# Performance work log

Hardware: AMD Instinct MI355X
Metric: run time of the kernel (lower is better)

Reference implementation:

```python
import jax, jax.numpy as jnp
import numpy as np

N_OBJ = 100000
E = 64
SMOOTH = 12.0  # MAXIMUM_SMOOTHNESS


def _mish(x):
    return x * jnp.tanh(jax.nn.softplus(x))


def _mlp(x, wi, bi, wo, bo):
    # torch.nn.Linear convention: y = x @ W.T + b
    return jnp.dot(_mish(jnp.dot(x, wi.T) + bi), wo.T) + bo


def _linear_init(key, out_dim, in_dim):
    s = 1.0 / np.sqrt(in_dim)
    kw, kb = jax.random.split(key)
    w = jax.random.uniform(kw, (out_dim, in_dim), jnp.float32, -s, s)
    b = jax.random.uniform(kb, (out_dim,), jnp.float32, -s, s)
    return w, b


def setup_inputs() -> dict:
    key = jax.random.key(0)
    ks = jax.random.split(key, 16)
    inp = {}
    inp["object_embeddings"] = jax.random.normal(ks[0], (N_OBJ, E), jnp.float32)
    inp["idx_unary"] = jax.random.randint(ks[1], (200000,), 0, N_OBJ, jnp.int32)
    inp["idx_binary"] = jax.random.randint(ks[2], (600000,), 0, N_OBJ, jnp.int32)
    inp["idx_ternary"] = jax.random.randint(ks[3], (300000,), 0, N_OBJ, jnp.int32)
    k = 4
    for name, ar in [("unary", 1), ("binary", 2), ("ternary", 3)]:
        d = ar * E
        wi, bi = _linear_init(ks[k], d, d)
        wo, bo = _linear_init(ks[k + 1], d, d)
        inp[f"{name}_wi"], inp[f"{name}_bi"] = wi, bi
        inp[f"{name}_wo"], inp[f"{name}_bo"] = wo, bo
        k += 2
    # update MLP: Linear(2E,2E) then Linear(2E,E)
    inp["upd_wi"], inp["upd_bi"] = _linear_init(ks[k], 2 * E, 2 * E)
    inp["upd_wo"], inp["upd_bo"] = _linear_init(ks[k + 1], E, 2 * E)
    return inp


def reference(object_embeddings, idx_unary, idx_binary, idx_ternary,
              unary_wi, unary_bi, unary_wo, unary_bo,
              binary_wi, binary_bi, binary_wo, binary_bo,
              ternary_wi, ternary_bi, ternary_wo, ternary_bo,
              upd_wi, upd_bi, upd_wo, upd_bo):
    def rel_msg(idx, arity, wi, bi, wo, bo):
        x = object_embeddings[idx].reshape(-1, arity * E)  # gather
        m = x + _mlp(x, wi, bi, wo, bo)                    # residual per-relation MLP
        return m.reshape(-1, E)

    msgs = jnp.concatenate([
        rel_msg(idx_unary, 1, unary_wi, unary_bi, unary_wo, unary_bo),
        rel_msg(idx_binary, 2, binary_wi, binary_bi, binary_wo, binary_bo),
        rel_msg(idx_ternary, 3, ternary_wi, ternary_bi, ternary_wo, ternary_bo),
    ], axis=0)
    inds = jnp.concatenate([idx_unary, idx_binary, idx_ternary], axis=0)

    # scatter-amax (include_self=False -> untouched rows stay 0, like torch zeros init)
    mx = jax.ops.segment_max(msgs, inds, num_segments=N_OBJ)
    mx = jnp.where(jnp.isneginf(mx), 0.0, mx)
    mx = jax.lax.stop_gradient(mx)

    exps = jnp.exp(SMOOTH * (msgs - mx[inds]))
    s = jax.ops.segment_sum(exps, inds, num_segments=N_OBJ) + 1e-16
    max_msg = jnp.log(s) / SMOOTH + mx  # smooth log-sum-exp aggregation

    upd_in = jnp.concatenate([max_msg, object_embeddings], axis=1)
    return object_embeddings + _mlp(upd_in, upd_wi, upd_bi, upd_wo, upd_bo)
```

## Files before the change

kernel.cpp:

```cpp
#include <hip/hip_runtime.h>
#include <math.h>

#define NOBJ 100000
#define SMOOTH 12.0f

typedef __attribute__((ext_vector_type(8))) short bf16x8;
typedef __attribute__((ext_vector_type(4))) float f32x4;
typedef unsigned short u16;
typedef unsigned int u32;
typedef unsigned long long u64;

#define OFF_UWI 0
#define OFF_UWO 4096
#define OFF_BWI 8192
#define OFF_BWO 24576
#define OFF_TWI 40960
#define OFF_TWO 77824
#define OFF_PWI 114688
#define OFF_PWO 131072
#define WTOT    139264
__device__ u16 g_wbf[WTOT];

__device__ __forceinline__ u16 f2b(float x) {
    union { float f; u32 u; } v; v.f = x;
    u32 r = v.u + 0x7FFFu + ((v.u >> 16) & 1);
    return (u16)(r >> 16);
}
__device__ __forceinline__ float b2f(u16 b) {
    union { u32 u; float f; } v; v.u = ((u32)b) << 16; return v.f;
}
__device__ __forceinline__ float mish_fast(float x) {
    float e = __expf(fminf(x, 15.f));
    float t = __builtin_fmaf(e, e, 2.f * e);
    return x * t * __builtin_amdgcn_rcpf(t + 2.f);
}
__device__ __forceinline__ double exp12_f64(float m) {
    float t = m * (SMOOTH * 1.4426950408889634f);
    float n = floorf(t);
    float f = exp2f(t - n);
    return ldexp((double)f, (int)n);
}
__device__ __forceinline__ float lse_from_sum(double S) {
    if (S == 0.0) return -3.0701134573253942f;
    union { double d; u64 u; } vu; vu.d = S;
    int k = (int)((vu.u >> 52) & 0x7FF) - 1022;
    vu.u = (vu.u & 0x000FFFFFFFFFFFFFULL) | 0x3FE0000000000000ULL;
    float fr = (float)vu.d;
    return ((float)k + __log2f(fr)) * 0.057762265046662105f;
}

__global__ void prep_kernel(const float* __restrict__ uwi, const float* __restrict__ uwo,
                            const float* __restrict__ bwi, const float* __restrict__ bwo,
                            const float* __restrict__ twi, const float* __restrict__ two_,
                            const float* __restrict__ pwi, const float* __restrict__ pwo,
                            const float* __restrict__ emb, u16* __restrict__ emb_bf,
                            u32* __restrict__ counts, u32* __restrict__ cursor) {
    int i = blockIdx.x * 256 + threadIdx.x;
    if (i < WTOT) {
        const float* src; int off;
        if      (i < OFF_UWO) { src = uwi; off = OFF_UWI; }
        else if (i < OFF_BWI) { src = uwo; off = OFF_UWO; }
        else if (i < OFF_BWO) { src = bwi; off = OFF_BWI; }
        else if (i < OFF_TWI) { src = bwo; off = OFF_BWO; }
        else if (i < OFF_TWO) { src = twi; off = OFF_TWI; }
        else if (i < OFF_PWI) { src = two_; off = OFF_TWO; }
        else if (i < OFF_PWO) { src = pwi; off = OFF_PWI; }
        else                  { src = pwo; off = OFF_PWO; }
        g_wbf[i] = f2b(src[i - off]);
    }
    if (i < NOBJ * 16) {
        float4 v = ((const float4*)emb)[i];
        ushort4 o;
        o.x = f2b(v.x); o.y = f2b(v.y); o.z = f2b(v.z); o.w = f2b(v.w);
        ((ushort4*)emb_bf)[i] = o;
    }
    if (counts && i < NOBJ) { counts[i] = 0u; cursor[i] = 0u; }
}

__device__ __forceinline__ int lookup_obj(long long m,
                                          const int* __restrict__ iu, int nU,
                                          const int* __restrict__ ib, int nB,
                                          const int* __restrict__ it) {
    if (m < nU) return iu[m];
    m -= nU;
    if (m < nB) return ib[m];
    return it[m - nB];
}

__global__ void hist_kernel(const int* __restrict__ iu, int nU,
                            const int* __restrict__ ib, int nB,
                            const int* __restrict__ it, int nT,
                            u32* __restrict__ counts) {
    long long t = (long long)blockIdx.x * 256 + threadIdx.x;
    if (t >= (long long)nU + nB + nT) return;
    atomicAdd(&counts[lookup_obj(t, iu, nU, ib, nB, it)], 1u);
}

__global__ void scan1_kernel(const u32* __restrict__ counts, u32* __restrict__ offs,
                             u32* __restrict__ bsum) {
    __shared__ u32 s[256];
    int t = threadIdx.x;
    int g = blockIdx.x * 256 + t;
    u32 v = (g < NOBJ) ? counts[g] : 0u;
    s[t] = v; __syncthreads();
    for (int off = 1; off < 256; off <<= 1) {
        u32 x = (t >= off) ? s[t - off] : 0u; __syncthreads();
        s[t] += x; __syncthreads();
    }
    if (g < NOBJ) offs[g] = s[t] - v;
    if (t == 255) bsum[blockIdx.x] = s[255];
}

__global__ void scan2_kernel(u32* __restrict__ bsum, int nblk) {
    __shared__ u32 s[512];
    int t = threadIdx.x;
    u32 v = (t < nblk) ? bsum[t] : 0u;
    s[t] = v; __syncthreads();
    for (int off = 1; off < 512; off <<= 1) {
        u32 x = (t >= off) ? s[t - off] : 0u; __syncthreads();
        s[t] += x; __syncthreads();
    }
    if (t < nblk) bsum[t] = s[t] - v;
}

__global__ void slot_kernel(const int* __restrict__ iu, int nU,
                            const int* __restrict__ ib, int nB,
                            const int* __restrict__ it, int nT,
                            const u32* __restrict__ offs, const u32* __restrict__ bsum,
                            u32* __restrict__ cursor, u32* __restrict__ slotByRef) {
    long long t = (long long)blockIdx.x * 256 + threadIdx.x;
    if (t >= (long long)nU + nB + nT) return;
    int obj = lookup_obj(t, iu, nU, ib, nB, it);
    u32 pos = atomicAdd(&cursor[obj], 1u);
    slotByRef[t] = offs[obj] + bsum[obj >> 8] + pos;
}

template<int D, int MW, int MODE, int WOFF_I, int WOFF_O>
__global__ __launch_bounds__(64 * MW)
void rel_pass_mfma(const u16* __restrict__ emb_bf,
                   const int* __restrict__ idx, int nRows,
                   const float* __restrict__ bi, const float* __restrict__ bo,
                   double* __restrict__ ssum64,
                   u16* __restrict__ msgs_out, const u32* __restrict__ slotByRef,
                   long long baseRef) {
    constexpr int ARITY = D / 64;
    constexpr int NT = D / 16;
    constexpr int NSC = D / 64;
    constexpr int M = MW * 16;
    __shared__ u16 xs[M * D];
    __shared__ u16 wlds[D * 64];
    __shared__ int objsm[M * ARITY];
    __shared__ u32 slotm[M * ARITY];

    const int tid = threadIdx.x;
    const int w = tid >> 6, l = tid & 63;
    const int lo = l & 15, hi = l >> 4;
    const int row0 = blockIdx.x * M;

    for (int i = tid; i < M * ARITY; i += 64 * MW) {
        int row = row0 + i / ARITY;
        bool ok = (row < nRows);
        objsm[i] = ok ? idx[(size_t)row * ARITY + i % ARITY] : -1;
        if (MODE == 3)
            slotm[i] = ok ? slotByRef[baseRef + (long long)row0 * ARITY + i] : 0xFFFFFFFFu;
    }
    __syncthreads();

    for (int i = tid; i < M * D / 8; i += 64 * MW) {
        int r = i / (D / 8), c8 = i % (D / 8);
        int obj = objsm[r * ARITY + (c8 >> 3)];
        bf16x8 v = {0, 0, 0, 0, 0, 0, 0, 0};
        if (obj >= 0) v = *(const bf16x8*)(emb_bf + (size_t)obj * 64 + (c8 & 7) * 8);
        *(bf16x8*)&xs[(r * D + c8 * 8) ^ ((r & 7) << 3)] = v;
    }

    f32x4 acc[NT];
    const int arow = w * 16 + lo;
    const int asw = (arow & 7) << 3;

#pragma unroll
    for (int n = 0; n < NT; ++n) { float b = bi[n * 16 + lo]; acc[n] = (f32x4){b, b, b, b}; }
#pragma unroll
    for (int sc = 0; sc < NSC; ++sc) {
        __syncthreads();
        for (int i = tid; i < D * 8; i += 64 * MW) {
            int u = i * 8;
            int j = u >> 6;
            bf16x8 v = *(const bf16x8*)&g_wbf[WOFF_I + j * D + sc * 64 + (u & 63)];
            *(bf16x8*)&wlds[u ^ ((j & 7) << 3)] = v;
        }
        __syncthreads();
#pragma unroll
        for (int kkL = 0; kkL < 2; ++kkL) {
            bf16x8 a = *(const bf16x8*)&xs[(arow * D + (sc * 2 + kkL) * 32 + hi * 8) ^ asw];
#pragma unroll
            for (int n = 0; n < NT; ++n) {
                int j = n * 16 + lo;
                bf16x8 b = *(const bf16x8*)&wlds[(j * 64 + kkL * 32 + hi * 8) ^ ((j & 7) << 3)];
                acc[n] = __builtin_amdgcn_mfma_f32_16x16x32_bf16(a, b, acc[n], 0, 0, 0);
            }
        }
    }

#pragma unroll
    for (int n = 0; n < NT; ++n) {
        float bov = bo[n * 16 + lo];
#pragma unroll
        for (int r = 0; r < 4; ++r) {
            int row = w * 16 + hi * 4 + r;
            int col = n * 16 + lo;
            int sidx = (row * D + col) ^ ((row & 7) << 3);
            float xv = b2f(xs[sidx]);
            xs[sidx] = f2b(mish_fast(acc[n][r]));
            acc[n][r] = bov + xv;
        }
    }

#pragma unroll
    for (int sc = 0; sc < NSC; ++sc) {
        __syncthreads();
        for (int i = tid; i < D * 8; i += 64 * MW) {
            int u = i * 8;
            int j = u >> 6;
            bf16x8 v = *(const bf16x8*)&g_wbf[WOFF_O + j * D + sc * 64 + (u & 63)];
            *(bf16x8*)&wlds[u ^ ((j & 7) << 3)] = v;
        }
        __syncthreads();
#pragma unroll
        for (int kkL = 0; kkL < 2; ++kkL) {
            bf16x8 a = *(const bf16x8*)&xs[(arow * D + (sc * 2 + kkL) * 32 + hi * 8) ^ asw];
#pragma unroll
            for (int n = 0; n < NT; ++n) {
                int j = n * 16 + lo;
                bf16x8 b = *(const bf16x8*)&wlds[(j * 64 + kkL * 32 + hi * 8) ^ ((j & 7) << 3)];
                acc[n] = __builtin_amdgcn_mfma_f32_16x16x32_bf16(a, b, acc[n], 0, 0, 0);
            }
        }
    }

    if (MODE == 3) {
#pragma unroll
        for (int n = 0; n < NT; ++n) {
            int col = n * 16 + lo;
#pragma unroll
            for (int r = 0; r < 4; ++r) {
                int row = w * 16 + hi * 4 + r;
                _Float16 hv = (_Float16)acc[n][r];
                xs[(row * D + col) ^ ((row & 7) << 3)] = *(u16*)&hv;
            }
        }
        __syncthreads();
        for (int i = tid; i < M * D / 8; i += 64 * MW) {
            int u = i * 8;
            int row = u / D, off = u - row * D;
            u32 slot = slotm[row * ARITY + (off >> 6)];
            if (slot == 0xFFFFFFFFu) continue;
            *(bf16x8*)(msgs_out + (size_t)slot * 64 + (off & 63)) =
                *(const bf16x8*)&xs[u ^ ((row & 7) << 3)];
        }
    } else {
#pragma unroll
        for (int n = 0; n < NT; ++n) {
            int col = n * 16 + lo;
#pragma unroll
            for (int r = 0; r < 4; ++r) {
                int row = w * 16 + hi * 4 + r;
                int obj = objsm[row * ARITY + (col >> 6)];
                if (obj < 0) continue;
                unsafeAtomicAdd(&ssum64[(size_t)obj * 64 + (col & 63)], exp12_f64(acc[n][r]));
            }
        }
    }
}

__global__ __launch_bounds__(256)
void agg_kernel(const u16* __restrict__ msgs,
                const u32* __restrict__ offs, const u32* __restrict__ bsum,
                const u32* __restrict__ counts,
                float* __restrict__ lse_out) {
    int o = blockIdx.x * 4 + (threadIdx.x >> 6);
    int l = threadIdx.x & 63;
    if (o >= NOBJ) return;
    u32 off = offs[o] + bsum[o >> 8];
    u32 n = counts[o];
    const u16* mrow = msgs + (size_t)off * 64 + l;
    double S0 = 0.0, S1 = 0.0, S2 = 0.0, S3 = 0.0;
    u32 j = 0;
    for (; j + 4 <= n; j += 4) {
        u16 h0 = mrow[(size_t)(j + 0) * 64];
        u16 h1 = mrow[(size_t)(j + 1) * 64];
        u16 h2 = mrow[(size_t)(j + 2) * 64];
        u16 h3 = mrow[(size_t)(j + 3) * 64];
        S0 += exp12_f64((float)(*(const _Float16*)&h0));
        S1 += exp12_f64((float)(*(const _Float16*)&h1));
        S2 += exp12_f64((float)(*(const _Float16*)&h2));
        S3 += exp12_f64((float)(*(const _Float16*)&h3));
    }
    for (; j < n; ++j) {
        u16 h = mrow[(size_t)j * 64];
        S0 += exp12_f64((float)(*(const _Float16*)&h));
    }
    lse_out[(size_t)o * 64 + l] = lse_from_sum((S0 + S1) + (S2 + S3));
}

__global__ __launch_bounds__(256)
void update_from_lse(const float* __restrict__ emb, const float* lsein,
                     const float* __restrict__ bi, const float* __restrict__ bo,
                     float* out) {
    __shared__ u16 uin[64 * 128];
    __shared__ u16 h[64 * 128];
    const int tid = threadIdx.x;
    const int w = tid >> 6, l = tid & 63, lo = l & 15, hi = l >> 4;
    const int row0 = blockIdx.x * 64;

    for (int i = tid; i < 64 * 128; i += 256) {
        int r = i >> 7, c = i & 127;
        int obj = row0 + r;
        float v = 0.f;
        if (obj < NOBJ) {
            if (c < 64) v = lsein[(size_t)obj * 64 + c];
            else v = emb[(size_t)obj * 64 + (c - 64)];
        }
        uin[i ^ ((r & 7) << 3)] = f2b(v);
    }
    __syncthreads();

    const int arow = w * 16 + lo;
    const int asw = (arow & 7) << 3;
    f32x4 acc[8];
#pragma unroll
    for (int n = 0; n < 8; ++n) { float b = bi[n * 16 + lo]; acc[n] = (f32x4){b, b, b, b}; }
#pragma unroll
    for (int kk = 0; kk < 4; ++kk) {
        bf16x8 a = *(const bf16x8*)&uin[(arow * 128 + kk * 32 + hi * 8) ^ asw];
#pragma unroll
        for (int n = 0; n < 8; ++n) {
            bf16x8 b = *(const bf16x8*)&g_wbf[OFF_PWI + (n * 16 + lo) * 128 + kk * 32 + hi * 8];
            acc[n] = __builtin_amdgcn_mfma_f32_16x16x32_bf16(a, b, acc[n], 0, 0, 0);
        }
    }
#pragma unroll
    for (int n = 0; n < 8; ++n) {
#pragma unroll
        for (int r = 0; r < 4; ++r) {
            int row = w * 16 + hi * 4 + r;
            int col = n * 16 + lo;
            h[(row * 128 + col) ^ ((row & 7) << 3)] = f2b(mish_fast(acc[n][r]));
        }
    }
    __syncthreads();
    f32x4 acc2[4];
#pragma unroll
    for (int n = 0; n < 4; ++n) { float b = bo[n * 16 + lo]; acc2[n] = (f32x4){b, b, b, b}; }
#pragma unroll
    for (int kk = 0; kk < 4; ++kk) {
        bf16x8 a = *(const bf16x8*)&h[(arow * 128 + kk * 32 + hi * 8) ^ asw];
#pragma unroll
        for (int n = 0; n < 4; ++n) {
            bf16x8 b = *(const bf16x8*)&g_wbf[OFF_PWO + (n * 16 + lo) * 128 + kk * 32 + hi * 8];
            acc2[n] = __builtin_amdgcn_mfma_f32_16x16x32_bf16(a, b, acc2[n], 0, 0, 0);
        }
    }
#pragma unroll
    for (int n = 0; n < 4; ++n) {
        int col = n * 16 + lo;
#pragma unroll
        for (int r = 0; r < 4; ++r) {
            int row = w * 16 + hi * 4 + r;
            int obj = row0 + row;
            if (obj < NOBJ)
                out[(size_t)obj * 64 + col] = emb[(size_t)obj * 64 + col] + acc2[n][r];
        }
    }
}

__global__ __launch_bounds__(256)
void update_mfma_f64(const float* __restrict__ emb, const double* __restrict__ ssum64,
                     const float* __restrict__ bi, const float* __restrict__ bo,
                     float* __restrict__ out) {
    __shared__ u16 uin[64 * 128];
    __shared__ u16 h[64 * 128];
    const int tid = threadIdx.x;
    const int w = tid >> 6, l = tid & 63, lo = l & 15, hi = l >> 4;
    const int row0 = blockIdx.x * 64;

    for (int i = tid; i < 64 * 128; i += 256) {
        int r = i >> 7, c = i & 127;
        int obj = row0 + r;
        float v = 0.f;
        if (obj < NOBJ) {
            if (c < 64) v = lse_from_sum(ssum64[(size_t)obj * 64 + c]);
            else v = emb[(size_t)obj * 64 + (c - 64)];
        }
        uin[i ^ ((r & 7) << 3)] = f2b(v);
    }
    __syncthreads();

    const int arow = w * 16 + lo;
    const int asw = (arow & 7) << 3;
    f32x4 acc[8];
#pragma unroll
    for (int n = 0; n < 8; ++n) { float b = bi[n * 16 + lo]; acc[n] = (f32x4){b, b, b, b}; }
#pragma unroll
    for (int kk = 0; kk < 4; ++kk) {
        bf16x8 a = *(const bf16x8*)&uin[(arow * 128 + kk * 32 + hi * 8) ^ asw];
#pragma unroll
        for (int n = 0; n < 8; ++n) {
            bf16x8 b = *(const bf16x8*)&g_wbf[OFF_PWI + (n * 16 + lo) * 128 + kk * 32 + hi * 8];
            acc[n] = __builtin_amdgcn_mfma_f32_16x16x32_bf16(a, b, acc[n], 0, 0, 0);
        }
    }
#pragma unroll
    for (int n = 0; n < 8; ++n) {
#pragma unroll
        for (int r = 0; r < 4; ++r) {
            int row = w * 16 + hi * 4 + r;
            int col = n * 16 + lo;
            h[(row * 128 + col) ^ ((row & 7) << 3)] = f2b(mish_fast(acc[n][r]));
        }
    }
    __syncthreads();
    f32x4 acc2[4];
#pragma unroll
    for (int n = 0; n < 4; ++n) { float b = bo[n * 16 + lo]; acc2[n] = (f32x4){b, b, b, b}; }
#pragma unroll
    for (int kk = 0; kk < 4; ++kk) {
        bf16x8 a = *(const bf16x8*)&h[(arow * 128 + kk * 32 + hi * 8) ^ asw];
#pragma unroll
        for (int n = 0; n < 4; ++n) {
            bf16x8 b = *(const bf16x8*)&g_wbf[OFF_PWO + (n * 16 + lo) * 128 + kk * 32 + hi * 8];
            acc2[n] = __builtin_amdgcn_mfma_f32_16x16x32_bf16(a, b, acc2[n], 0, 0, 0);
        }
    }
#pragma unroll
    for (int n = 0; n < 4; ++n) {
        int col = n * 16 + lo;
#pragma unroll
        for (int r = 0; r < 4; ++r) {
            int row = w * 16 + hi * 4 + r;
            int obj = row0 + row;
            if (obj < NOBJ)
                out[(size_t)obj * 64 + col] = emb[(size_t)obj * 64 + col] + acc2[n][r];
        }
    }
}

static inline size_t align256(size_t x) { return (x + 255) & ~(size_t)255; }

extern "C" void kernel_launch(void* const* d_in, const int* in_sizes, int n_in,
                              void* d_out, int out_size, void* d_ws, size_t ws_size,
                              hipStream_t stream) {
    const float* emb = (const float*)d_in[0];
    const int* iu = (const int*)d_in[1];
    const int* ib = (const int*)d_in[2];
    const int* it = (const int*)d_in[3];
    const float* uwi = (const float*)d_in[4];
    const float* ubi = (const float*)d_in[5];
    const float* uwo = (const float*)d_in[6];
    const float* ubo = (const float*)d_in[7];
    const float* bwi = (const float*)d_in[8];
    const float* bbi = (const float*)d_in[9];
    const float* bwo = (const float*)d_in[10];
    const float* bbo = (const float*)d_in[11];
    const float* twi = (const float*)d_in[12];
    const float* tbi = (const float*)d_in[13];
    const float* two_ = (const float*)d_in[14];
    const float* tbo = (const float*)d_in[15];
    const float* pwi = (const float*)d_in[16];
    const float* pbi = (const float*)d_in[17];
    const float* pwo = (const float*)d_in[18];
    const float* pbo = (const float*)d_in[19];

    const int nU = in_sizes[1];
    const int nB = in_sizes[2];
    const int nT = in_sizes[3];
    const int rowsU = nU;
    const int rowsB = nB / 2;
    const int rowsT = nT / 3;
    const long long NREF = (long long)nU + nB + nT;

    const size_t seg = (size_t)NOBJ * 64;
    const int gU = (rowsU + 127) / 128;
    const int gB = (rowsB + 127) / 128;
    const int gT = (rowsT + 127) / 128;
    const int nblkScan = (NOBJ + 255) / 256;
    const int gPrep = (NOBJ * 16 + 255) / 256;

    char* p = (char*)d_ws;
    u16* msgs = (u16*)p;        p += align256(2 * (size_t)NREF * 64);
    u32* counts = (u32*)p;      p += align256(4 * (size_t)NOBJ);
    u32* offs = (u32*)p;        p += align256(4 * (size_t)NOBJ);
    u32* cursor = (u32*)p;      p += align256(4 * (size_t)NOBJ);
    u32* bsum = (u32*)p;        p += align256(4 * 512);
    u32* slotByRef = (u32*)p;   p += align256(4 * (size_t)NREF);
    u16* emb_bf = (u16*)p;      p += align256(2 * seg);
    const size_t need = (size_t)(p - (char*)d_ws);

    if (ws_size >= need) {
        prep_kernel<<<gPrep, 256, 0, stream>>>(uwi, uwo, bwi, bwo, twi, two_, pwi, pwo,
                                               emb, emb_bf, counts, cursor);
        int gRef = (int)((NREF + 255) / 256);
        hist_kernel<<<gRef, 256, 0, stream>>>(iu, nU, ib, nB, it, nT, counts);
        scan1_kernel<<<nblkScan, 256, 0, stream>>>(counts, offs, bsum);
        scan2_kernel<<<1, 512, 0, stream>>>(bsum, nblkScan);
        slot_kernel<<<gRef, 256, 0, stream>>>(iu, nU, ib, nB, it, nT, offs, bsum, cursor, slotByRef);

        rel_pass_mfma<64, 8, 3, OFF_UWI, OFF_UWO><<<gU, 512, 0, stream>>>(
            emb_bf, iu, rowsU, ubi, ubo, nullptr, msgs, slotByRef, 0LL);
        rel_pass_mfma<128, 8, 3, OFF_BWI, OFF_BWO><<<gB, 512, 0, stream>>>(
            emb_bf, ib, rowsB, bbi, bbo, nullptr, msgs, slotByRef, (long long)nU);
        rel_pass_mfma<192, 8, 3, OFF_TWI, OFF_TWO><<<gT, 512, 0, stream>>>(
            emb_bf, it, rowsT, tbi, tbo, nullptr, msgs, slotByRef, (long long)(nU + nB));

        float* lsebuf = (float*)d_out;
        agg_kernel<<<(NOBJ + 3) / 4, 256, 0, stream>>>(msgs, offs, bsum, counts, lsebuf);
        update_from_lse<<<(NOBJ + 63) / 64, 256, 0, stream>>>(
            emb, lsebuf, pbi, pbo, (float*)d_out);
    } else {
        double* ssum64 = (double*)d_ws;
        u16* emb_bf2 = (u16*)((char*)d_ws + seg * sizeof(double));
        prep_kernel<<<gPrep, 256, 0, stream>>>(uwi, uwo, bwi, bwo, twi, two_, pwi, pwo,
                                               emb, emb_bf2, nullptr, nullptr);
        hipMemsetAsync(ssum64, 0, seg * sizeof(double), stream);
        rel_pass_mfma<64, 8, 2, OFF_UWI, OFF_UWO><<<gU, 512, 0, stream>>>(
            emb_bf2, iu, rowsU, ubi, ubo, ssum64, nullptr, nullptr, 0);
        rel_pass_mfma<128, 8, 2, OFF_BWI, OFF_BWO><<<gB, 512, 0, stream>>>(
            emb_bf2, ib, rowsB, bbi, bbo, ssum64, nullptr, nullptr, 0);
        rel_pass_mfma<192, 8, 2, OFF_TWI, OFF_TWO><<<gT, 512, 0, stream>>>(
            emb_bf2, it, rowsT, tbi, tbo, ssum64, nullptr, nullptr, 0);
        update_mfma_f64<<<(NOBJ + 63) / 64, 256, 0, stream>>>(
            emb, ssum64, pbi, pbo, (float*)d_out);
    }
}
```

Measured before the change: 361.5 us.

## Double-buffer weight tiles in LDS with register prefetch in relation MLP kernel

Weight K-slices in the relation-pass MFMA kernel are now staged through two 32-column LDS buffers, and the global loads for the next slices are prefetched into registers while the current slice is multiplied. This replaces the old pattern of load, barrier, compute per 64-column chunk, which had two barriers and exposed global load latency each time. The first and second GEMMs run in one unified stage loop, with the mish and residual step placed at the boundary. It costs more registers, which may lower occupancy, and the swizzle changes to a 32-wide row layout.

```diff
diff --git a/kernel.cpp b/kernel.cpp
--- a/kernel.cpp
+++ b/kernel.cpp
@@ -5,6 +5,7 @@
 #define SMOOTH 12.0f
 
 typedef __attribute__((ext_vector_type(8))) short bf16x8;
+typedef __attribute__((ext_vector_type(4))) short bf16x4;
 typedef __attribute__((ext_vector_type(4))) float f32x4;
 typedef unsigned short u16;
 typedef unsigned int u32;
@@ -135,6 +136,24 @@
     slotByRef[t] = offs[obj] + bsum[obj >> 8] + pos;
 }
 
+#define LOADW(s_, reg_) do {                                                   \
+    const int woff_ = ((s_) < KT) ? WOFF_I : WOFF_O;                           \
+    const int cs_ = ((s_) < KT) ? (s_) : (s_) - KT;                            \
+    _Pragma("unroll")                                                          \
+    for (int q = 0; q < NCH; ++q) {                                            \
+        int o_ = (tid + q * NTHR) * 4;                                         \
+        int j_ = o_ >> 5, c_ = o_ & 31;                                        \
+        reg_[q] = *(const bf16x4*)&g_wbf[woff_ + j_ * D + cs_ * 32 + c_];      \
+    } } while (0)
+
+#define WRITEW(buf_, reg_) do {                                                \
+    _Pragma("unroll")                                                          \
+    for (int q = 0; q < NCH; ++q) {                                            \
+        int o_ = (tid + q * NTHR) * 4;                                         \
+        int j_ = o_ >> 5, c_ = o_ & 31;                                        \
+        *(bf16x4*)&wlds[buf_][(j_ * 32 + c_) ^ ((j_ & 3) << 3)] = reg_[q];     \
+    } } while (0)
+
 template<int D, int MW, int MODE, int WOFF_I, int WOFF_O>
 __global__ __launch_bounds__(64 * MW)
 void rel_pass_mfma(const u16* __restrict__ emb_bf,
@@ -145,10 +164,13 @@
                    long long baseRef) {
     constexpr int ARITY = D / 64;
     constexpr int NT = D / 16;
-    constexpr int NSC = D / 64;
+    constexpr int KT = D / 32;
+    constexpr int ST = 2 * KT;
     constexpr int M = MW * 16;
+    constexpr int NTHR = 64 * MW;
+    constexpr int NCH = D * 32 / 4 / NTHR;
     __shared__ u16 xs[M * D];
-    __shared__ u16 wlds[D * 64];
+    __shared__ u16 wlds[2][D * 32];
     __shared__ int objsm[M * ARITY];
     __shared__ u32 slotm[M * ARITY];
 
@@ -157,85 +179,69 @@
     const int lo = l & 15, hi = l >> 4;
     const int row0 = blockIdx.x * M;
 
-    for (int i = tid; i < M * ARITY; i += 64 * MW) {
+    bf16x4 wrA[NCH], wrB[NCH];
+
+    for (int i = tid; i < M * ARITY; i += NTHR) {
         int row = row0 + i / ARITY;
         bool ok = (row < nRows);
         objsm[i] = ok ? idx[(size_t)row * ARITY + i % ARITY] : -1;
         if (MODE == 3)
             slotm[i] = ok ? slotByRef[baseRef + (long long)row0 * ARITY + i] : 0xFFFFFFFFu;
     }
+    LOADW(0, wrA);
+    LOADW(1, wrB);
     __syncthreads();
 
-    for (int i = tid; i < M * D / 8; i += 64 * MW) {
+    for (int i = tid; i < M * D / 8; i += NTHR) {
         int r = i / (D / 8), c8 = i % (D / 8);
         int obj = objsm[r * ARITY + (c8 >> 3)];
         bf16x8 v = {0, 0, 0, 0, 0, 0, 0, 0};
         if (obj >= 0) v = *(const bf16x8*)(emb_bf + (size_t)obj * 64 + (c8 & 7) * 8);
         *(bf16x8*)&xs[(r * D + c8 * 8) ^ ((r & 7) << 3)] = v;
     }
+    WRITEW(0, wrA);
+    __syncthreads();
 
     f32x4 acc[NT];
     const int arow = w * 16 + lo;
     const int asw = (arow & 7) << 3;
-
 #pragma unroll
     for (int n = 0; n < NT; ++n) { float b = bi[n * 16 + lo]; acc[n] = (f32x4){b, b, b, b}; }
-#pragma unroll
-    for (int sc = 0; sc < NSC; ++sc) {
-        __syncthreads();
-        for (int i = tid; i < D * 8; i += 64 * MW) {
-            int u = i * 8;
-            int j = u >> 6;
-            bf16x8 v = *(const bf16x8*)&g_wbf[WOFF_I + j * D + sc * 64 + (u & 63)];
-            *(bf16x8*)&wlds[u ^ ((j & 7) << 3)] = v;
-        }
-        __syncthreads();
-#pragma unroll
-        for (int kkL = 0; kkL < 2; ++kkL) {
-            bf16x8 a = *(const bf16x8*)&xs[(arow * D + (sc * 2 + kkL) * 32 + hi * 8) ^ asw];
+
+#pragma unroll
+    for (int s = 0; s < ST; ++s) {
+        if (s + 2 < ST) {
+            if (s & 1) { LOADW(s + 2, wrB); } else { LOADW(s + 2, wrA); }
+        }
+        if (s + 1 < ST) {
+            if (s & 1) { WRITEW((s + 1) & 1, wrA); } else { WRITEW((s + 1) & 1, wrB); }
+        }
+        {
+            const int kk = (s < KT) ? s : s - KT;
+            bf16x8 a = *(const bf16x8*)&xs[(arow * D + kk * 32 + hi * 8) ^ asw];
 #pragma unroll
             for (int n = 0; n < NT; ++n) {
                 int j = n * 16 + lo;
-                bf16x8 b = *(const bf16x8*)&wlds[(j * 64 + kkL * 32 + hi * 8) ^ ((j & 7) << 3)];
+                bf16x8 b = *(const bf16x8*)&wlds[s & 1][(j * 32 + hi * 8) ^ ((j & 3) << 3)];
                 acc[n] = __builtin_amdgcn_mfma_f32_16x16x32_bf16(a, b, acc[n], 0, 0, 0);
             }
         }
-    }
-
-#pragma unroll
-    for (int n = 0; n < NT; ++n) {
-        float bov = bo[n * 16 + lo];
-#pragma unroll
-        for (int r = 0; r < 4; ++r) {
-            int row = w * 16 + hi * 4 + r;
-            int col = n * 16 + lo;
-            int sidx = (row * D + col) ^ ((row & 7) << 3);
-            float xv = b2f(xs[sidx]);
-            xs[sidx] = f2b(mish_fast(acc[n][r]));
-            acc[n][r] = bov + xv;
-        }
-    }
-
-#pragma unroll
-    for (int sc = 0; sc < NSC; ++sc) {
+        if (s == KT - 1) {
+#pragma unroll
+            for (int n = 0; n < NT; ++n) {
+                float bov = bo[n * 16 + lo];
+#pragma unroll
+                for (int r = 0; r < 4; ++r) {
+                    int row = w * 16 + hi * 4 + r;
+                    int col = n * 16 + lo;
+                    int sidx = (row * D + col) ^ ((row & 7) << 3);
+                    float xv = b2f(xs[sidx]);
+                    xs[sidx] = f2b(mish_fast(acc[n][r]));
+                    acc[n][r] = bov + xv;
+                }
+            }
+        }
         __syncthreads();
-        for (int i = tid; i < D * 8; i += 64 * MW) {
-            int u = i * 8;
-            int j = u >> 6;
-            bf16x8 v = *(const bf16x8*)&g_wbf[WOFF_O + j * D + sc * 64 + (u & 63)];
-            *(bf16x8*)&wlds[u ^ ((j & 7) << 3)] = v;
-        }
-        __syncthreads();
-#pragma unroll
-        for (int kkL = 0; kkL < 2; ++kkL) {
-            bf16x8 a = *(const bf16x8*)&xs[(arow * D + (sc * 2 + kkL) * 32 + hi * 8) ^ asw];
-#pragma unroll
-            for (int n = 0; n < NT; ++n) {
-                int j = n * 16 + lo;
-                bf16x8 b = *(const bf16x8*)&wlds[(j * 64 + kkL * 32 + hi * 8) ^ ((j & 7) << 3)];
-                acc[n] = __builtin_amdgcn_mfma_f32_16x16x32_bf16(a, b, acc[n], 0, 0, 0);
-            }
-        }
     }
 
     if (MODE == 3) {
@@ -250,7 +256,7 @@
             }
         }
         __syncthreads();
-        for (int i = tid; i < M * D / 8; i += 64 * MW) {
+        for (int i = tid; i < M * D / 8; i += NTHR) {
             int u = i * 8;
             int row = u / D, off = u - row * D;
             u32 slot = slotm[row * ARITY + (off >> 6)];
```

Result: faster. 351.8 us (-2.7%).
